# Kernel tuning notes

Measured on AMD Instinct MI355X. Metric: run time of the kernel, lower is better.

## Reference

```python
import jax, jax.numpy as jnp
import numpy as np

C = 384          # hardcoded input dim in Head
H = 6            # num_heads
D = 64           # head_size (H*D == C)

def setup_inputs() -> dict:
    key = jax.random.key(0)
    ks = jax.random.split(key, 6)
    x = jax.random.normal(ks[0], (4, 2048, C), dtype=jnp.float32)
    # per-head projection weights stacked: [H, C, D]
    s = 1.0 / np.sqrt(C)
    Wq = jax.random.uniform(ks[1], (H, C, D), minval=-s, maxval=s, dtype=jnp.float32)
    Wk = jax.random.uniform(ks[2], (H, C, D), minval=-s, maxval=s, dtype=jnp.float32)
    Wv = jax.random.uniform(ks[3], (H, C, D), minval=-s, maxval=s, dtype=jnp.float32)
    sp = 1.0 / np.sqrt(H * D)
    Wo = jax.random.uniform(ks[4], (H * D, H * D), minval=-sp, maxval=sp, dtype=jnp.float32)
    bo = jax.random.uniform(ks[5], (H * D,), minval=-sp, maxval=sp, dtype=jnp.float32)
    return {"x": x, "Wq": Wq, "Wk": Wk, "Wv": Wv, "Wo": Wo, "bo": bo}

def reference(x, Wq, Wk, Wv, Wo, bo):
    B, T, _ = x.shape
    # per-head projections (batched over heads instead of a Python loop)
    q = jnp.einsum('btc,hcd->bhtd', x, Wq)
    k = jnp.einsum('btc,hcd->bhtd', x, Wk)
    v = jnp.einsum('btc,hcd->bhtd', x, Wv)
    scale = 1.0 / jnp.sqrt(jnp.asarray(D, dtype=x.dtype))
    scores = jnp.einsum('bhtd,bhsd->bhts', q, k) * scale  # [B,H,T,T]
    attn = jax.nn.softmax(scores, axis=-1)                # no causal mask in source
    out = jnp.einsum('bhts,bhsd->bhtd', attn, v)          # [B,H,T,D]
    # concat heads: [B,T,H*D] (head order matches torch.cat over heads)
    out = out.transpose(0, 2, 1, 3).reshape(B, T, H * D)
    return out @ Wo + bo
```

## Files before the change

### kernel.cpp

```cpp
#include <hip/hip_runtime.h>

typedef unsigned short u16;
typedef float  f32x4 __attribute__((ext_vector_type(4)));
typedef short  s16x8 __attribute__((ext_vector_type(8)));
typedef unsigned int u32x2 __attribute__((ext_vector_type(2)));
typedef unsigned int u32x4 __attribute__((ext_vector_type(4)));

union U8 { u32x4 u; u32x2 u2[2]; s16x8 s; };

__device__ __forceinline__ u16 f2bs(float f) {
    union { float f; unsigned int u; } x; x.f = f;
    return (u16)((x.u + 0x7FFFu + ((x.u >> 16) & 1u)) >> 16);
}

#if __has_builtin(__builtin_amdgcn_exp2f)
#define EXP2(v) __builtin_amdgcn_exp2f(v)
#else
#define EXP2(v) exp2f(v)
#endif

__device__ __forceinline__ f32x4 mfma16(s16x8 a, s16x8 b, f32x4 c) {
    return __builtin_amdgcn_mfma_f32_16x16x32_bf16(a, b, c, 0, 0, 0);
}

typedef __attribute__((address_space(3))) unsigned int lds_u32;
typedef const __attribute__((address_space(1))) unsigned int glb_u32;
__device__ __forceinline__ void gl16(const u16* g, u16* l) {
    __builtin_amdgcn_global_load_lds((glb_u32*)g, (lds_u32*)l, 16, 0, 0);
}

__global__ __launch_bounds__(256) void pack_w2(const float* __restrict__ Wq,
                                               const float* __restrict__ Wk,
                                               const float* __restrict__ Wv,
                                               const float* __restrict__ Wo,
                                               u16* __restrict__ Wt) {
    __shared__ float tile[64][65];
    const int bid = blockIdx.x, tid = threadIdx.x;
    const float* src; u16* dst; int src_ld, sr0, sc0;
    if (bid < 108) {
        int tensor = bid / 36, rem = bid % 36, h = rem / 6, ct = rem % 6;
        const float* W = (tensor == 0) ? Wq : (tensor == 1) ? Wk : Wv;
        src = W + h * 24576; src_ld = 64; sr0 = ct * 64; sc0 = 0;
        dst = Wt + tensor * 147456 + h * 24576;
    } else {
        int rem = bid - 108, et = rem / 6, ft = rem % 6;
        src = Wo; src_ld = 384; sr0 = ft * 64; sc0 = et * 64;
        dst = Wt + 3 * 147456;
    }
    const int r = tid >> 2, cb = (tid & 3) * 16;
    const float* sp = src + (size_t)(sr0 + r) * src_ld + sc0 + cb;
    #pragma unroll
    for (int j = 0; j < 4; ++j)
        *(f32x4*)&tile[r][cb + j * 4] = *(const f32x4*)(sp + j * 4);
    __syncthreads();
    struct alignas(16) OV { u16 v[16]; } ov;
    #pragma unroll
    for (int j = 0; j < 16; ++j) ov.v[j] = f2bs(tile[cb + j][r]);
    u16* dp = dst + (size_t)(sc0 + r) * 384 + sr0 + cb;
    *(u32x4*)dp       = *(u32x4*)&ov.v[0];
    *(u32x4*)(dp + 8) = *(u32x4*)&ov.v[8];
}

__global__ __launch_bounds__(256) void convert_x(const float* __restrict__ x, u16* __restrict__ xb) {
    const int i = (blockIdx.x * 256 + threadIdx.x) * 8;
    f32x4 a = *(const f32x4*)(x + i);
    f32x4 b = *(const f32x4*)(x + i + 4);
    U8 o;
    #pragma unroll
    for (int j = 0; j < 4; ++j) { o.s[j] = (short)f2bs(a[j]); o.s[4 + j] = (short)f2bs(b[j]); }
    *(u32x4*)(xb + i) = o.u;
}

__global__ __launch_bounds__(256) void proj2(const u16* __restrict__ xb,
                                             const u16* __restrict__ Wt,
                                             u16* __restrict__ Qb,
                                             u16* __restrict__ Kb,
                                             u16* __restrict__ Vb) {
    __shared__ u16 As[2][128 * 32];
    __shared__ u16 Bs[2][128 * 32];
    const int tid = threadIdx.x, w = tid >> 6, lane = tid & 63;
    const int lr = lane & 15, lg = lane >> 4;
    const int wr = w >> 1, wc = w & 1;
    const int mt = blockIdx.x, nt = blockIdx.y;
    const int m0 = mt * 128, n0 = nt * 128;

    const int c0 = w * 2 * 64 + lane;
    const int ar0 = c0 >> 2, acc0 = c0 & 3;
    const int c1 = c0 + 64;
    const int ar1 = c1 >> 2, acc1 = c1 & 3;
    const u16* gA0 = xb + (size_t)(m0 + ar0) * 384 + acc0 * 8;
    const u16* gA1 = xb + (size_t)(m0 + ar1) * 384 + acc1 * 8;
    const u16* gB0 = Wt + (size_t)(n0 + ar0) * 384 + acc0 * 8;
    const u16* gB1 = Wt + (size_t)(n0 + ar1) * 384 + acc1 * 8;

    f32x4 acc[4][4];
    #pragma unroll
    for (int i = 0; i < 4; ++i)
        #pragma unroll
        for (int j = 0; j < 4; ++j) acc[i][j] = f32x4{0.f, 0.f, 0.f, 0.f};

    gl16(gA0, &As[0][(w * 2 + 0) * 512]);
    gl16(gA1, &As[0][(w * 2 + 1) * 512]);
    gl16(gB0, &Bs[0][(w * 2 + 0) * 512]);
    gl16(gB1, &Bs[0][(w * 2 + 1) * 512]);
    __syncthreads();

    for (int kt = 0; kt < 12; ++kt) {
        const int buf = kt & 1;
        if (kt < 11) {
            const int ko = (kt + 1) * 32;
            gl16(gA0 + ko, &As[buf ^ 1][(w * 2 + 0) * 512]);
            gl16(gA1 + ko, &As[buf ^ 1][(w * 2 + 1) * 512]);
            gl16(gB0 + ko, &Bs[buf ^ 1][(w * 2 + 0) * 512]);
            gl16(gB1 + ko, &Bs[buf ^ 1][(w * 2 + 1) * 512]);
        }
        U8 af[4], bf[4];
        #pragma unroll
        for (int f = 0; f < 4; ++f) {
            af[f].u = *(const u32x4*)&As[buf][(wr * 64 + f * 16 + lr) * 32 + lg * 8];
            bf[f].u = *(const u32x4*)&Bs[buf][(wc * 64 + f * 16 + lr) * 32 + lg * 8];
        }
        #pragma unroll
        for (int mf = 0; mf < 4; ++mf)
            #pragma unroll
            for (int nf = 0; nf < 4; ++nf)
                acc[mf][nf] = mfma16(af[mf].s, bf[nf].s, acc[mf][nf]);
        __syncthreads();
    }

    const int tensor = nt / 3;
    u16* dst = (tensor == 0) ? Qb : (tensor == 1) ? Kb : Vb;
    const float scl = (tensor == 0) ? 0.18033688011112042f : 1.0f;
    const int head_base = (nt % 3) * 2 + wc;
    #pragma unroll
    for (int mf = 0; mf < 4; ++mf)
        #pragma unroll
        for (int nf = 0; nf < 4; ++nf)
            #pragma unroll
            for (int r = 0; r < 4; ++r) {
                int m = m0 + wr * 64 + mf * 16 + lg * 4 + r;
                int b = m >> 11, t = m & 2047;
                int d = nf * 16 + lr;
                dst[((size_t)(b * 6 + head_base) * 2048 + t) * 64 + d] = f2bs(acc[mf][nf][r] * scl);
            }
}

__global__ __launch_bounds__(256) void transpose_v(const u16* __restrict__ Vb,
                                                   u16* __restrict__ Vt) {
    __shared__ u16 tile[64][72];
    const int bh = blockIdx.y, t0 = blockIdx.x * 64;
    const int tid = threadIdx.x;
    const int r = tid >> 2, c0 = (tid & 3) * 16;
    const u16* src = Vb + ((size_t)bh * 2048 + t0 + r) * 64 + c0;
    u32x4 a  = *(const u32x4*)(src);
    u32x4 b2 = *(const u32x4*)(src + 8);
    *(u32x4*)&tile[r][c0]     = a;
    *(u32x4*)&tile[r][c0 + 8] = b2;
    __syncthreads();
    struct alignas(16) OutV { u16 v[16]; } ov;
    #pragma unroll
    for (int j = 0; j < 16; ++j) ov.v[j] = tile[c0 + j][r];
    u16* dst = Vt + ((size_t)bh * 64 + r) * 2048 + t0 + c0;
    *(u32x4*)dst       = *(u32x4*)&ov.v[0];
    *(u32x4*)(dst + 8) = *(u32x4*)&ov.v[8];
}

__global__ __launch_bounds__(256) void attn_kernel(const u16* __restrict__ Qb,
                                                   const u16* __restrict__ Kb,
                                                   const u16* __restrict__ Vt,
                                                   u16* __restrict__ AO) {
    __shared__ char smem[16384];
    const int tid = threadIdx.x, w = tid >> 6, lane = tid & 63;
    const int lr = lane & 15, lg = lane >> 4;
    const int qt = blockIdx.x, bh = blockIdx.y;
    const int b = bh / 6, h = bh - b * 6;
    const int qbase = qt * 64 + w * 16;

    const u16* qp = Qb + ((size_t)bh * 2048 + qbase + lr) * 64 + lg * 8;
    U8 bq0, bq1;
    bq0.u = *(const u32x4*)qp;
    bq1.u = *(const u32x4*)(qp + 32);

    const int kkey = w * 8 + (lane >> 3);
    const int kchunk = lane & 7;
    const u16* ksrc = Kb + ((size_t)bh * 2048 + kkey) * 64 + kchunk * 8;
    const int kdst = kkey * 128 + ((kchunk ^ (kkey & 7)) * 16);
    const int vd = w * 16 + (lane >> 2);
    const int vs = lane & 3;
    const u16* vsrc = Vt + ((size_t)bh * 64 + vd) * 2048 + vs * 8;
    const int vdst = vd * 64 + ((vs ^ (vd & 3)) * 16);

    const int kb0 = lr * 128 + ((lg ^ (lr & 7)) * 16);
    const int kb1 = lr * 128 + (((lg + 4) ^ (lr & 7)) * 16);
    const int vlo = ((lg >> 1) ^ (lr & 3)) * 16 + (lg & 1) * 8;
    const int vhi = (((lg >> 1) + 2) ^ (lr & 3)) * 16 + (lg & 1) * 8;

    f32x4 acc[4];
    #pragma unroll
    for (int i = 0; i < 4; ++i) acc[i] = f32x4{0.f, 0.f, 0.f, 0.f};
    float rsum = 0.f;

    {
        u32x4 kreg = *(const u32x4*)ksrc;
        u32x4 vreg = *(const u32x4*)vsrc;
        ksrc += 2048; vsrc += 32;
        *(u32x4*)(smem + kdst) = kreg;
        *(u32x4*)(smem + 4096 + vdst) = vreg;
    }
    __syncthreads();

    for (int it = 0; it < 64; ++it) {
        const int buf = it & 1;
        const bool last = (it == 63);
        u32x4 knext, vnext;
        if (!last) {
            knext = *(const u32x4*)ksrc;
            vnext = *(const u32x4*)vsrc;
            ksrc += 2048; vsrc += 32;
        }
        const char* kbase = smem + buf * 8192;
        const char* vbase = kbase + 4096;

        U8 ak00, ak01, ak10, ak11;
        ak00.u = *(const u32x4*)(kbase + kb0);
        ak01.u = *(const u32x4*)(kbase + kb1);
        ak10.u = *(const u32x4*)(kbase + 2048 + kb0);
        ak11.u = *(const u32x4*)(kbase + 2048 + kb1);

        const f32x4 z{0.f, 0.f, 0.f, 0.f};
        f32x4 s0 = mfma16(ak00.s, bq0.s, z); s0 = mfma16(ak01.s, bq1.s, s0);
        f32x4 s1 = mfma16(ak10.s, bq0.s, z); s1 = mfma16(ak11.s, bq1.s, s1);

        float p[8];
        #pragma unroll
        for (int r = 0; r < 4; ++r) {
            p[r]     = EXP2(s0[r]);
            p[4 + r] = EXP2(s1[r]);
            rsum += p[r] + p[4 + r];
        }
        U8 pa;
        #pragma unroll
        for (int j = 0; j < 8; ++j) pa.s[j] = (short)f2bs(p[j]);

        #pragma unroll
        for (int dt = 0; dt < 4; ++dt) {
            const char* vrow = vbase + (dt * 16 + lr) * 64;
            U8 bv;
            bv.u2[0] = *(const u32x2*)(vrow + vlo);
            bv.u2[1] = *(const u32x2*)(vrow + vhi);
            acc[dt] = mfma16(pa.s, bv.s, acc[dt]);
        }

        if (!last) {
            char* nb = smem + (buf ^ 1) * 8192;
            *(u32x4*)(nb + kdst) = knext;
            *(u32x4*)(nb + 4096 + vdst) = vnext;
        }
        __syncthreads();
    }

    rsum += __shfl_xor(rsum, 16, 64);
    rsum += __shfl_xor(rsum, 32, 64);

    const size_t aobase = ((size_t)b * 2048 + qbase) * 384 + h * 64;
    #pragma unroll
    for (int r = 0; r < 4; ++r) {
        float inv = 1.0f / __shfl(rsum, lg * 4 + r, 64);
        #pragma unroll
        for (int dt = 0; dt < 4; ++dt)
            AO[aobase + (size_t)(lg * 4 + r) * 384 + dt * 16 + lr] = f2bs(acc[dt][r] * inv);
    }
}

__global__ __launch_bounds__(256) void outproj2(const u16* __restrict__ AO,
                                                const u16* __restrict__ Wot,
                                                const float* __restrict__ bo,
                                                float* __restrict__ out) {
    __shared__ u16 As[2][64 * 32];
    __shared__ u16 Bs[2][64 * 32];
    const int tid = threadIdx.x, w = tid >> 6, lane = tid & 63;
    const int lr = lane & 15, lg = lane >> 4;
    const int wr = w >> 1, wc = w & 1;
    const int mt = blockIdx.x, nt = blockIdx.y;
    const int m0 = mt * 64, n0 = nt * 64;

    const int c0 = w * 64 + lane;
    const int ar0 = c0 >> 2, cc0 = c0 & 3;
    const u16* gA = AO  + (size_t)(m0 + ar0) * 384 + cc0 * 8;
    const u16* gB = Wot + (size_t)(n0 + ar0) * 384 + cc0 * 8;

    f32x4 acc[2][2];
    #pragma unroll
    for (int i = 0; i < 2; ++i)
        #pragma unroll
        for (int j = 0; j < 2; ++j) acc[i][j] = f32x4{0.f, 0.f, 0.f, 0.f};

    gl16(gA, &As[0][w * 512]);
    gl16(gB, &Bs[0][w * 512]);
    __syncthreads();

    for (int kt = 0; kt < 12; ++kt) {
        const int buf = kt & 1;
        if (kt < 11) {
            const int ko = (kt + 1) * 32;
            gl16(gA + ko, &As[buf ^ 1][w * 512]);
            gl16(gB + ko, &Bs[buf ^ 1][w * 512]);
        }
        U8 af[2], bf[2];
        #pragma unroll
        for (int f = 0; f < 2; ++f) {
            af[f].u = *(const u32x4*)&As[buf][(wr * 32 + f * 16 + lr) * 32 + lg * 8];
            bf[f].u = *(const u32x4*)&Bs[buf][(wc * 32 + f * 16 + lr) * 32 + lg * 8];
        }
        #pragma unroll
        for (int mf = 0; mf < 2; ++mf)
            #pragma unroll
            for (int nf = 0; nf < 2; ++nf)
                acc[mf][nf] = mfma16(af[mf].s, bf[nf].s, acc[mf][nf]);
        __syncthreads();
    }

    #pragma unroll
    for (int mf = 0; mf < 2; ++mf)
        #pragma unroll
        for (int nf = 0; nf < 2; ++nf) {
            int col = n0 + wc * 32 + nf * 16 + lr;
            float bias = bo[col];
            #pragma unroll
            for (int r = 0; r < 4; ++r) {
                int m = m0 + wr * 32 + mf * 16 + lg * 4 + r;
                out[(size_t)m * 384 + col] = acc[mf][nf][r] + bias;
            }
        }
}

extern "C" void kernel_launch(void* const* d_in, const int* in_sizes, int n_in,
                              void* d_out, int out_size, void* d_ws, size_t ws_size,
                              hipStream_t stream) {
    const float* x  = (const float*)d_in[0];
    const float* Wq = (const float*)d_in[1];
    const float* Wk = (const float*)d_in[2];
    const float* Wv = (const float*)d_in[3];
    const float* Wo = (const float*)d_in[4];
    const float* bo = (const float*)d_in[5];
    float* out = (float*)d_out;
    char* ws = (char*)d_ws;

    u16* Wt  = (u16*)(ws);
    u16* Wot = (u16*)(ws + 884736);
    u16* xb  = (u16*)(ws + 1179648);
    u16* Qb  = (u16*)(ws + 7471104);
    u16* Kb  = (u16*)(ws + 13762560);
    u16* Vb  = (u16*)(ws + 20054016);
    u16* Vt  = (u16*)(ws + 26345472);
    u16* AO  = (u16*)(ws + 1179648);

    pack_w2<<<144, 256, 0, stream>>>(Wq, Wk, Wv, Wo, Wt);
    convert_x<<<1536, 256, 0, stream>>>(x, xb);
    proj2<<<dim3(64, 9), 256, 0, stream>>>(xb, Wt, Qb, Kb, Vb);
    transpose_v<<<dim3(32, 24), 256, 0, stream>>>(Vb, Vt);
    attn_kernel<<<dim3(32, 24), 256, 0, stream>>>(Qb, Kb, Vt, AO);
    outproj2<<<dim3(128, 6), 256, 0, stream>>>(AO, Wot, bo, out);
}
```

Measured before the change: 168.8 us.

## Rewrite attention loop with direct global-to-LDS loads and 64-key tiles

The attention kernel now loads K and V tiles straight from global memory into LDS with global_load_lds, replacing the register-staged copies. Each iteration processes 64 keys instead of 32, which halves the loop trip count and the number of barriers, and doubles the LDS buffers to 32 KB. Probabilities are packed to bf16 with the hardware v_cvt_pk_bf16_f32 instruction in place of the manual rounding. The aim is to cut per-iteration overhead and VGPR traffic, at the cost of more LDS per block, which may lower occupancy.

```diff
diff --git a/kernel.cpp b/kernel.cpp
--- a/kernel.cpp
+++ b/kernel.cpp
@@ -6,11 +6,17 @@
 typedef unsigned int u32x2 __attribute__((ext_vector_type(2)));
 typedef unsigned int u32x4 __attribute__((ext_vector_type(4)));
 
-union U8 { u32x4 u; u32x2 u2[2]; s16x8 s; };
+union U8 { u32x4 u; u32x2 u2[2]; s16x8 s; unsigned int uw[4]; };
 
 __device__ __forceinline__ u16 f2bs(float f) {
     union { float f; unsigned int u; } x; x.f = f;
     return (u16)((x.u + 0x7FFFu + ((x.u >> 16) & 1u)) >> 16);
+}
+
+__device__ __forceinline__ unsigned int cvtpk(float a, float b) {
+    unsigned int r;
+    asm("v_cvt_pk_bf16_f32 %0, %1, %2" : "=v"(r) : "v"(a), "v"(b));
+    return r;
 }
 
 #if __has_builtin(__builtin_amdgcn_exp2f)
@@ -165,11 +171,11 @@
     *(u32x4*)(dst + 8) = *(u32x4*)&ov.v[8];
 }
 
-__global__ __launch_bounds__(256) void attn_kernel(const u16* __restrict__ Qb,
-                                                   const u16* __restrict__ Kb,
-                                                   const u16* __restrict__ Vt,
-                                                   u16* __restrict__ AO) {
-    __shared__ char smem[16384];
+__global__ __launch_bounds__(256) void attn3(const u16* __restrict__ Qb,
+                                             const u16* __restrict__ Kb,
+                                             const u16* __restrict__ Vt,
+                                             u16* __restrict__ AO) {
+    __shared__ char smem[32768];
     const int tid = threadIdx.x, w = tid >> 6, lane = tid & 63;
     const int lr = lane & 15, lg = lane >> 4;
     const int qt = blockIdx.x, bh = blockIdx.y;
@@ -181,80 +187,78 @@
     bq0.u = *(const u32x4*)qp;
     bq1.u = *(const u32x4*)(qp + 32);
 
-    const int kkey = w * 8 + (lane >> 3);
-    const int kchunk = lane & 7;
-    const u16* ksrc = Kb + ((size_t)bh * 2048 + kkey) * 64 + kchunk * 8;
-    const int kdst = kkey * 128 + ((kchunk ^ (kkey & 7)) * 16);
-    const int vd = w * 16 + (lane >> 2);
-    const int vs = lane & 3;
-    const u16* vsrc = Vt + ((size_t)bh * 64 + vd) * 2048 + vs * 8;
-    const int vdst = vd * 64 + ((vs ^ (vd & 3)) * 16);
-
-    const int kb0 = lr * 128 + ((lg ^ (lr & 7)) * 16);
-    const int kb1 = lr * 128 + (((lg + 4) ^ (lr & 7)) * 16);
-    const int vlo = ((lg >> 1) ^ (lr & 3)) * 16 + (lg & 1) * 8;
-    const int vhi = (((lg >> 1) + 2) ^ (lr & 3)) * 16 + (lg & 1) * 8;
+    const int srow = lane >> 3;
+    const int slot = lane & 7;
+    const int chunk = slot ^ srow;
+    const u16* kg0 = Kb + (size_t)bh * 2048 * 64 + (size_t)(w * 16 + srow) * 64 + chunk * 8;
+    const u16* kg1 = kg0 + 8 * 64;
+    const u16* vg0 = Vt + (size_t)bh * 64 * 2048 + (size_t)(w * 16 + srow) * 2048 + chunk * 8;
+    const u16* vg1 = vg0 + 8 * 2048;
+
+    const int rx = lr & 7;
+    const int kOffA = lr * 128 + ((lg ^ rx) * 16);
+    const int kOffB = lr * 128 + (((4 + lg) ^ rx) * 16);
+    const int vRow = lr * 128 + (lg & 1) * 8;
+    const int vC = lg >> 1;
 
     f32x4 acc[4];
     #pragma unroll
     for (int i = 0; i < 4; ++i) acc[i] = f32x4{0.f, 0.f, 0.f, 0.f};
     float rsum = 0.f;
 
-    {
-        u32x4 kreg = *(const u32x4*)ksrc;
-        u32x4 vreg = *(const u32x4*)vsrc;
-        ksrc += 2048; vsrc += 32;
-        *(u32x4*)(smem + kdst) = kreg;
-        *(u32x4*)(smem + 4096 + vdst) = vreg;
-    }
-    __syncthreads();
-
-    for (int it = 0; it < 64; ++it) {
+    gl16(kg0, (u16*)(smem + w * 2048));
+    gl16(kg1, (u16*)(smem + w * 2048 + 1024));
+    gl16(vg0, (u16*)(smem + 8192 + w * 2048));
+    gl16(vg1, (u16*)(smem + 8192 + w * 2048 + 1024));
+    kg0 += 4096; kg1 += 4096; vg0 += 64; vg1 += 64;
+    __syncthreads();
+
+    for (int it = 0; it < 32; ++it) {
         const int buf = it & 1;
-        const bool last = (it == 63);
-        u32x4 knext, vnext;
-        if (!last) {
-            knext = *(const u32x4*)ksrc;
-            vnext = *(const u32x4*)vsrc;
-            ksrc += 2048; vsrc += 32;
-        }
-        const char* kbase = smem + buf * 8192;
-        const char* vbase = kbase + 4096;
-
-        U8 ak00, ak01, ak10, ak11;
-        ak00.u = *(const u32x4*)(kbase + kb0);
-        ak01.u = *(const u32x4*)(kbase + kb1);
-        ak10.u = *(const u32x4*)(kbase + 2048 + kb0);
-        ak11.u = *(const u32x4*)(kbase + 2048 + kb1);
-
+        const char* kbase = smem + buf * 16384;
+        const char* vbase = kbase + 8192;
+
+        if (it < 31) {
+            char* nb = smem + (buf ^ 1) * 16384;
+            gl16(kg0, (u16*)(nb + w * 2048));
+            gl16(kg1, (u16*)(nb + w * 2048 + 1024));
+            gl16(vg0, (u16*)(nb + 8192 + w * 2048));
+            gl16(vg1, (u16*)(nb + 8192 + w * 2048 + 1024));
+            kg0 += 4096; kg1 += 4096; vg0 += 64; vg1 += 64;
+        }
+
+        float p[16];
         const f32x4 z{0.f, 0.f, 0.f, 0.f};
-        f32x4 s0 = mfma16(ak00.s, bq0.s, z); s0 = mfma16(ak01.s, bq1.s, s0);
-        f32x4 s1 = mfma16(ak10.s, bq0.s, z); s1 = mfma16(ak11.s, bq1.s, s1);
-
-        float p[8];
-        #pragma unroll
-        for (int r = 0; r < 4; ++r) {
-            p[r]     = EXP2(s0[r]);
-            p[4 + r] = EXP2(s1[r]);
-            rsum += p[r] + p[4 + r];
-        }
-        U8 pa;
-        #pragma unroll
-        for (int j = 0; j < 8; ++j) pa.s[j] = (short)f2bs(p[j]);
+        #pragma unroll
+        for (int t = 0; t < 4; ++t) {
+            U8 ak0, ak1;
+            ak0.u = *(const u32x4*)(kbase + t * 2048 + kOffA);
+            ak1.u = *(const u32x4*)(kbase + t * 2048 + kOffB);
+            f32x4 s = mfma16(ak0.s, bq0.s, z);
+            s = mfma16(ak1.s, bq1.s, s);
+            #pragma unroll
+            for (int r = 0; r < 4; ++r) p[t * 4 + r] = EXP2(s[r]);
+        }
+        #pragma unroll
+        for (int i = 0; i < 16; ++i) rsum += p[i];
+
+        U8 pa0, pa1;
+        #pragma unroll
+        for (int i = 0; i < 4; ++i) {
+            pa0.uw[i] = cvtpk(p[2 * i],     p[2 * i + 1]);
+            pa1.uw[i] = cvtpk(p[8 + 2 * i], p[9 + 2 * i]);
+        }
 
         #pragma unroll
         for (int dt = 0; dt < 4; ++dt) {
-            const char* vrow = vbase + (dt * 16 + lr) * 64;
-            U8 bv;
-            bv.u2[0] = *(const u32x2*)(vrow + vlo);
-            bv.u2[1] = *(const u32x2*)(vrow + vhi);
-            acc[dt] = mfma16(pa.s, bv.s, acc[dt]);
-        }
-
-        if (!last) {
-            char* nb = smem + (buf ^ 1) * 8192;
-            *(u32x4*)(nb + kdst) = knext;
-            *(u32x4*)(nb + 4096 + vdst) = vnext;
+            const char* vr = vbase + dt * 2048 + vRow;
+            U8 bv0, bv1;
+            bv0.u2[0] = *(const u32x2*)(vr + (((0 + vC) ^ rx) << 4));
+            bv0.u2[1] = *(const u32x2*)(vr + (((2 + vC) ^ rx) << 4));
+            bv1.u2[0] = *(const u32x2*)(vr + (((4 + vC) ^ rx) << 4));
+            bv1.u2[1] = *(const u32x2*)(vr + (((6 + vC) ^ rx) << 4));
+            acc[dt] = mfma16(pa0.s, bv0.s, acc[dt]);
+            acc[dt] = mfma16(pa1.s, bv1.s, acc[dt]);
         }
         __syncthreads();
     }
@@ -359,6 +363,6 @@
     convert_x<<<1536, 256, 0, stream>>>(x, xb);
     proj2<<<dim3(64, 9), 256, 0, stream>>>(xb, Wt, Qb, Kb, Vb);
     transpose_v<<<dim3(32, 24), 256, 0, stream>>>(Vb, Vt);
-    attn_kernel<<<dim3(32, 24), 256, 0, stream>>>(Qb, Kb, Vt, AO);
+    attn3<<<dim3(32, 24), 256, 0, stream>>>(Qb, Kb, Vt, AO);
     outproj2<<<dim3(128, 6), 256, 0, stream>>>(AO, Wot, bo, out);
 }
```

Result: faster. 145.9 us (-13.6%).
